# Kernel tuning notes

Hardware: AMD Instinct MI355X
Metric: run time of the kernel (lower is better)

Reference implementation:

```python
import jax, jax.numpy as jnp
import numpy as np

# Static config (matches init_kwargs)
B = 1
D = 1024          # model_dim
H = 16            # num_heads
HD = 64           # head_dim
TPF = 256         # tokens_per_frame = latent_height*latent_width
LH, LW = 16, 16
FRAMES = 13
PREFIX = 1
ATTN = 3
CHUNKS = 4
TXT = 226                 # text_length per chunk
SEQ_TXT = CHUNKS * TXT    # 904
VID_LEN = FRAMES * TPF    # 3328
CHUNK_VID = (PREFIX + ATTN) * TPF  # 1024 video tokens per attention chunk
THETA = 10000.0
EPS = 1e-6
SCALE = 1.0 / np.sqrt(HD)
DT, DHE, DW = 16, 24, 24  # 3D rope split of head_dim


def setup_inputs() -> dict:
    key = jax.random.key(0)
    ks = jax.random.split(key, 16)
    def w(k, shape, s=0.02):
        return (jax.random.normal(k, shape) * s).astype(jnp.float32)
    return dict(
        vid_emb=jax.random.normal(ks[0], (B, VID_LEN, D), jnp.float32),
        text_emb=jax.random.normal(ks[1], (B, SEQ_TXT, D), jnp.float32),
        Wq=w(ks[2], (D, D)), bq=jnp.zeros((D,), jnp.float32),
        Wk=w(ks[3], (D, D)), bk=jnp.zeros((D,), jnp.float32),
        Wv=w(ks[4], (D, D)), bv=jnp.zeros((D,), jnp.float32),
        Wo=w(ks[5], (D, D)), bo=jnp.zeros((D,), jnp.float32),
        qn_w=jnp.ones((HD,), jnp.float32), qn_b=jnp.zeros((HD,), jnp.float32),
        kn_w=jnp.ones((HD,), jnp.float32), kn_b=jnp.zeros((HD,), jnp.float32),
        ssm_Win=w(ks[6], (D, D)), ssm_Wout=w(ks[7], (D, D)),
        ssm_gate=jnp.zeros((D,), jnp.float32),
        fg_t=jnp.full((D,), 0.1, jnp.float32), fg_v=jnp.full((D,), 0.1, jnp.float32),
        bg_t=jnp.full((D,), 0.1, jnp.float32), bg_v=jnp.full((D,), 0.1, jnp.float32),
    )


def _layernorm(x, w, b):
    mu = jnp.mean(x, axis=-1, keepdims=True)
    var = jnp.mean((x - mu) ** 2, axis=-1, keepdims=True)
    return (x - mu) * jax.lax.rsqrt(var + EPS) * w + b


def _rope_angles():
    # per-video-token 3D positions within a chunk
    tok = jnp.arange(CHUNK_VID)
    f = (tok // TPF).astype(jnp.float32)
    rem = tok % TPF
    hp = (rem // LW).astype(jnp.float32)
    wp = (rem % LW).astype(jnp.float32)
    def inv(d):
        return THETA ** (-jnp.arange(0, d, 2, dtype=jnp.float32) / d)
    return f[:, None] * inv(DT), hp[:, None] * inv(DHE), wp[:, None] * inv(DW)


def _rot(x, ang):
    half = x.shape[-1] // 2
    c, s = jnp.cos(ang), jnp.sin(ang)
    x1, x2 = x[..., :half], x[..., half:]
    return jnp.concatenate([x1 * c - x2 * s, x1 * s + x2 * c], axis=-1)


def _apply_rope3d(x, angs):
    at, ah, aw = angs
    return jnp.concatenate([
        _rot(x[..., :DT], at),
        _rot(x[..., DT:DT + DHE], ah),
        _rot(x[..., DT + DHE:], aw),
    ], axis=-1)


def _attn_forward(vid_emb, text_emb, Wq, bq, Wk, bk, Wv, bv, Wo, bo, qn_w, qn_b, kn_w, kn_b):
    b = vid_emb.shape[0]
    starts = np.arange(CHUNKS) * ATTN * TPF
    idx = jnp.asarray(starts)[:, None] + jnp.arange(CHUNK_VID)[None, :]  # [C, CHUNK_VID]
    txt_chunks = text_emb.reshape(b, CHUNKS, TXT, D)
    vid_chunks = vid_emb[:, idx]                                          # [b, C, CHUNK_VID, D]
    cur = jnp.concatenate([txt_chunks, vid_chunks], axis=2)               # [b, C, T, D]
    T = TXT + CHUNK_VID
    cur = cur.reshape(b * CHUNKS, T, D)

    def heads(x):
        return x.reshape(b * CHUNKS, T, H, HD).transpose(0, 2, 1, 3)      # [bc, h, t, d]

    q = _layernorm(heads(cur @ Wq + bq), qn_w, qn_b)
    k = _layernorm(heads(cur @ Wk + bk), kn_w, kn_b)
    v = heads(cur @ Wv + bv)

    angs = _rope_angles()
    q = jnp.concatenate([q[:, :, :TXT], _apply_rope3d(q[:, :, TXT:], angs)], axis=2)
    k = jnp.concatenate([k[:, :, :TXT], _apply_rope3d(k[:, :, TXT:], angs)], axis=2)

    scores = jnp.einsum('bhqd,bhkd->bhqk', q, k) * SCALE
    attn = jax.nn.softmax(scores, axis=-1)
    out = jnp.einsum('bhqk,bhkd->bhqd', attn, v)
    out = out.transpose(0, 2, 1, 3).reshape(b * CHUNKS, T, D) @ Wo + bo
    out = out.reshape(b, CHUNKS, T, D)

    text_out = out[:, :, :TXT].reshape(b, SEQ_TXT, D)
    vid_part = out[:, :, TXT:]                                            # [b, C, CHUNK_VID, D]
    vid_acc = jnp.zeros((b, VID_LEN, D), vid_emb.dtype).at[:, idx].add(vid_part)
    cnt = jnp.zeros((b, VID_LEN, 1), vid_emb.dtype).at[:, idx].add(jnp.ones((b, CHUNKS, CHUNK_VID, 1), vid_emb.dtype))
    vid_out = vid_acc / cnt
    return jnp.concatenate([text_out, vid_out], axis=1)


def _ssm(x, Win, Wout, gate_logit):
    # simplified TTT stand-in: gated linear recurrence h_t = g*h_{t-1} + u_t (causal scan)
    g = jax.nn.sigmoid(gate_logit)
    u = x @ Win
    a = jnp.broadcast_to(g, u.shape)
    def comb(c1, c2):
        a1, b1 = c1
        a2, b2 = c2
        return a1 * a2, a2 * b1 + b2
    _, h = jax.lax.associative_scan(comb, (a, u), axis=1)
    return h @ Wout


def _rev_text_chunks(t):
    b = t.shape[0]
    return jnp.flip(t.reshape(b, CHUNKS, TXT, D), axis=1).reshape(b, SEQ_TXT, D)


def _ssm_forward(emb, ssm_Win, ssm_Wout, ssm_gate, fg_t, fg_v, bg_t, bg_v):
    Ttxt = SEQ_TXT
    res = emb
    y = _ssm(emb, ssm_Win, ssm_Wout, ssm_gate)
    emb = res + jnp.concatenate([jnp.tanh(fg_t) * y[:, :Ttxt], jnp.tanh(fg_v) * y[:, Ttxt:]], axis=1)
    res2 = emb
    # multiscene reverse: flip text chunk order and video token order
    rev = jnp.concatenate([_rev_text_chunks(emb[:, :Ttxt]), jnp.flip(emb[:, Ttxt:], axis=1)], axis=1)
    y2 = _ssm(rev, ssm_Win, ssm_Wout, ssm_gate)
    y2 = jnp.concatenate([_rev_text_chunks(y2[:, :Ttxt]), jnp.flip(y2[:, Ttxt:], axis=1)], axis=1)
    return res2 + jnp.concatenate([jnp.tanh(bg_t) * y2[:, :Ttxt], jnp.tanh(bg_v) * y2[:, Ttxt:]], axis=1)


def reference(vid_emb, text_emb, Wq, bq, Wk, bk, Wv, bv, Wo, bo, qn_w, qn_b, kn_w, kn_b,
              ssm_Win, ssm_Wout, ssm_gate, fg_t, fg_v, bg_t, bg_v):
    emb = _attn_forward(vid_emb, text_emb, Wq, bq, Wk, bk, Wv, bv, Wo, bo, qn_w, qn_b, kn_w, kn_b)
    out = _ssm_forward(emb, ssm_Win, ssm_Wout, ssm_gate, fg_t, fg_v, bg_t, bg_v)
    return out[:, SEQ_TXT:], out[:, :SEQ_TXT]
```

## Files before the change

kernel.cpp:

```cpp
#include <hip/hip_runtime.h>
#include <cstdint>

constexpr int Dm       = 1024;
constexpr int Hh       = 16;
constexpr int HD       = 64;
constexpr int CHUNKS   = 4;
constexpr int TXT      = 226;
constexpr int SEQ_TXT  = 904;
constexpr int VID_LEN  = 3328;
constexpr int CHUNK_VID= 1024;
constexpr int Tt       = 1250;
constexpr int Tp       = 1280;
constexpr int M_QKV    = 5000;
constexpr int SEQm     = 4232;
constexpr int STRIDE_V = 768;
constexpr float EPSc   = 1e-6f;
constexpr float SCALEc = 0.125f;
constexpr float OFFS   = 8.0f;
constexpr float C16    = 1.6609640474f;
constexpr float C24    = 1.1073093649f;

constexpr int SEGL2 = 64;
constexpr int HALO  = 64;
constexpr int NSEG2 = (SEQm + SEGL2 - 1) / SEGL2;

typedef __attribute__((ext_vector_type(8))) short bf16x8;
typedef __attribute__((ext_vector_type(4))) float f32x4;

__device__ __forceinline__ ushort f2bf(float x) {
    uint32_t u = __float_as_uint(x);
    u += 0x7FFFu + ((u >> 16) & 1u);
    return (ushort)(u >> 16);
}
__device__ __forceinline__ float bf2f(ushort b) {
    return __uint_as_float(((uint32_t)b) << 16);
}

__device__ __forceinline__ void gload_lds16(const ushort* g, ushort* l) {
    __builtin_amdgcn_global_load_lds(
        (const __attribute__((address_space(1))) unsigned int*)g,
        (__attribute__((address_space(3))) unsigned int*)l, 16, 0, 0);
}

__device__ __forceinline__ int rev_map(int i) {
    if (i < SEQ_TXT) {
        int c = i / TXT, o = i - c * TXT;
        return (CHUNKS - 1 - c) * TXT + o;
    }
    int j = i - SEQ_TXT;
    return SEQ_TXT + (VID_LEN - 1 - j);
}

__global__ __launch_bounds__(256) void prep_all(
    const float* __restrict__ Wq, const float* __restrict__ Wk,
    const float* __restrict__ Wv, const float* __restrict__ Wo,
    const float* __restrict__ Win, const float* __restrict__ Wout,
    const float* __restrict__ vid, const float* __restrict__ txt,
    ushort* __restrict__ WqkvH, ushort* __restrict__ WqkvL,
    ushort* __restrict__ WoH, ushort* __restrict__ WoL,
    ushort* __restrict__ WinH, ushort* __restrict__ WinL,
    ushort* __restrict__ WoutH, ushort* __restrict__ WoutL,
    ushort* __restrict__ chi, ushort* __restrict__ clo) {
    __shared__ float tile[32][33];
    if (blockIdx.z == 6) {
        int base = (blockIdx.y * 32 + blockIdx.x) * 256 + threadIdx.x;
        for (int idx = base; idx < M_QKV * 256; idx += 32 * 32 * 256) {
            int row = idx >> 8, c4 = (idx & 255) * 4;
            int c = row / Tt, t = row - c * Tt;
            float4 x;
            if (t < TXT)
                x = *(const float4*)(txt + (size_t)(c * TXT + t) * Dm + c4);
            else
                x = *(const float4*)(vid + (size_t)(c * STRIDE_V + (t - TXT)) * Dm + c4);
            float v[4] = {x.x, x.y, x.z, x.w};
            ushort4 h, l;
            h.x = f2bf(v[0]); l.x = f2bf(v[0] - bf2f(h.x));
            h.y = f2bf(v[1]); l.y = f2bf(v[1] - bf2f(h.y));
            h.z = f2bf(v[2]); l.z = f2bf(v[2] - bf2f(h.z));
            h.w = f2bf(v[3]); l.w = f2bf(v[3] - bf2f(h.w));
            *(ushort4*)(chi + (size_t)row * Dm + c4) = h;
            *(ushort4*)(clo + (size_t)row * Dm + c4) = l;
        }
        return;
    }
    const float* W; ushort* Thi; ushort* Tlo;
    switch (blockIdx.z) {
        case 0: W = Wq;  Thi = WqkvH;               Tlo = WqkvL;               break;
        case 1: W = Wk;  Thi = WqkvH + 1024*1024;   Tlo = WqkvL + 1024*1024;   break;
        case 2: W = Wv;  Thi = WqkvH + 2*1024*1024; Tlo = WqkvL + 2*1024*1024; break;
        case 3: W = Wo;  Thi = WoH;   Tlo = WoL;   break;
        case 4: W = Win; Thi = WinH;  Tlo = WinL;  break;
        default:W = Wout;Thi = WoutH; Tlo = WoutL; break;
    }
    int k0 = blockIdx.y * 32, n0 = blockIdx.x * 32;
    int j = threadIdx.x & 31, i0 = threadIdx.x >> 5;
#pragma unroll
    for (int i = i0; i < 32; i += 8)
        tile[i][j] = W[(size_t)(k0 + i) * 1024 + n0 + j];
    __syncthreads();
#pragma unroll
    for (int i = i0; i < 32; i += 8) {
        float v = tile[j][i];
        ushort h = f2bf(v);
        size_t o = (size_t)(n0 + i) * 1024 + k0 + j;
        Thi[o] = h;
        Tlo[o] = f2bf(v - bf2f(h));
    }
}

template<int MODE>
__global__ __launch_bounds__(256) void gemm_sk(
    const ushort* __restrict__ Ahi, const ushort* __restrict__ Alo,
    const ushort* __restrict__ Bhi, const ushort* __restrict__ Blo,
    const float* __restrict__ f1, const float* __restrict__ f2,
    const float* __restrict__ f3,
    float* __restrict__ Cf, ushort* __restrict__ u1,
    int M, int N) {
    __shared__ ushort AHL[128 * 64];
    __shared__ ushort BHL[128 * 64];
    const int tid = threadIdx.x;
    const int w = tid >> 6, lane = tid & 63;
    const int lrow = lane & 15, quad = lane >> 4;
    const int mBase = blockIdx.y * 128, nBase = blockIdx.x * 128;

    const bool isB = (w >= 2);
    const int half = w & 1;
    const ushort* Phi = isB ? Bhi : Ahi;
    const ushort* Plo = isB ? Blo : Alo;
    ushort* lds = (isB ? BHL : AHL) + half * 4096;
    const int baseR = (isB ? nBase : mBase) + half * 64;
    const int maxr = (isB ? N : M) - 1;
    const int rl8 = lane >> 3;
    const int c = (lane & 7) ^ rl8;
    const ushort* Psel = (c < 4) ? Phi : Plo;
    const ushort* gb[8];
#pragma unroll
    for (int u = 0; u < 8; ++u) {
        int rg = min(baseR + u * 8 + rl8, maxr);
        gb[u] = Psel + (size_t)rg * 1024 + (c & 3) * 8;
    }

    const int mo = (w >> 1) * 64, no = (w & 1) * 64;
    const int p = quad ^ (lrow & 7);
    f32x4 acc[4][4];
#pragma unroll
    for (int i = 0; i < 4; ++i)
#pragma unroll
        for (int j = 0; j < 4; ++j) acc[i][j] = (f32x4){0.f, 0.f, 0.f, 0.f};

    const int kk0 = (MODE == 5) ? blockIdx.z * 512 : 0;
    const int kk1 = (MODE == 5) ? kk0 + 512 : 1024;
    for (int kk = kk0; kk < kk1; kk += 32) {
        __syncthreads();
#pragma unroll
        for (int u = 0; u < 8; ++u) gload_lds16(gb[u] + kk, lds + u * 512);
        __syncthreads();

        bf16x8 ah[4], al[4], bh[4], bl[4];
#pragma unroll
        for (int i = 0; i < 4; ++i) {
            int m = mo + i * 16 + lrow;
            ah[i] = *(const bf16x8*)&AHL[m * 64 + p * 8];
            al[i] = *(const bf16x8*)&AHL[m * 64 + (p ^ 4) * 8];
        }
#pragma unroll
        for (int j = 0; j < 4; ++j) {
            int n = no + j * 16 + lrow;
            bh[j] = *(const bf16x8*)&BHL[n * 64 + p * 8];
            bl[j] = *(const bf16x8*)&BHL[n * 64 + (p ^ 4) * 8];
        }
#pragma unroll
        for (int i = 0; i < 4; ++i)
#pragma unroll
            for (int j = 0; j < 4; ++j) {
                f32x4 a = acc[i][j];
                a = __builtin_amdgcn_mfma_f32_16x16x32_bf16(ah[i], bh[j], a, 0, 0, 0);
                a = __builtin_amdgcn_mfma_f32_16x16x32_bf16(al[i], bh[j], a, 0, 0, 0);
                a = __builtin_amdgcn_mfma_f32_16x16x32_bf16(ah[i], bl[j], a, 0, 0, 0);
                acc[i][j] = a;
            }
    }

    const size_t zoff = (MODE == 5) ? (size_t)blockIdx.z * M * N : 0;
#pragma unroll
    for (int i = 0; i < 4; ++i)
#pragma unroll
        for (int j = 0; j < 4; ++j) {
            const int col = nBase + no + j * 16 + lrow;
            float bv = 0.f;
            if constexpr (MODE == 1)
                bv = (col < 1024) ? f1[col]
                   : (col < 2048) ? f2[col - 1024] : f3[col - 2048];
#pragma unroll
            for (int r = 0; r < 4; ++r) {
                const int row = mBase + mo + i * 16 + quad * 4 + r;
                if (row >= M) continue;
                const size_t idx = (size_t)row * N + col;
                const float a = acc[i][j][r];
                if constexpr (MODE == 1) {
                    u1[idx] = f2bf(a + bv);
                } else {
                    Cf[zoff + idx] = a;
                }
            }
        }
}

__global__ __launch_bounds__(512, 2) void gemm_qkv_8ph(
    const ushort* __restrict__ Ahi, const ushort* __restrict__ Alo,
    const ushort* __restrict__ Bhi, const ushort* __restrict__ Blo,
    const float* __restrict__ f1, const float* __restrict__ f2,
    const float* __restrict__ f3, ushort* __restrict__ out) {
    constexpr int Mq  = M_QKV;
    constexpr int Nq  = 3072;
    constexpr int NKT = 48;

    __shared__ __align__(16) ushort sA00[8192], sA01[8192];
    __shared__ __align__(16) ushort sA10[8192], sA11[8192];
    __shared__ __align__(16) ushort sB00[8192], sB01[8192];
    __shared__ __align__(16) ushort sB10[8192], sB11[8192];

    const int tid = threadIdx.x;
    const int w = tid >> 6, lane = tid & 63;
    const int lrow = lane & 15, quad = lane >> 4;
    const int wr = w >> 2, wc = w & 3;

    const int wg  = blockIdx.y * 12 + blockIdx.x;
    const int swz = (wg & 7) * 30 + (wg >> 3);
    const int bx  = swz % 12, by = swz / 12;
    const int mBase = by * 256, nBase = bx * 256;

    uint32_t offA[2][2], offB[2][2];
#pragma unroll
    for (int q = 0; q < 2; ++q) {
        const int s  = q * 512 + tid;
        const int sr = s >> 3;
        const int c  = (s & 7) ^ (sr & 7);
        const int ra = (sr >> 6) * 128 + (sr & 63);
        const int rb = (sr >> 5) * 64 + (sr & 31);
#pragma unroll
        for (int h = 0; h < 2; ++h) {
            offA[q][h] = (uint32_t)(min(mBase + ra + h * 64, Mq - 1) * 1024 + c * 8);
            offB[q][h] = (uint32_t)((nBase + rb + h * 32) * 1024 + c * 8);
        }
    }
    const int ldsW = w * 512;

    const int pA0 = quad ^ (lrow & 7);
    const int pA1 = (4 + quad) ^ (lrow & 7);
    const int arow = wr * 64 + lrow;
    const int brow = wc * 32 + lrow;

    f32x4 acc[8][4];
#pragma unroll
    for (int i = 0; i < 8; ++i)
#pragma unroll
        for (int j = 0; j < 4; ++j) acc[i][j] = (f32x4){0.f, 0.f, 0.f, 0.f};

    bf16x8 af[8];
    bf16x8 bfX[4];
    bf16x8 bfY[4];

#define STAGE_A(b, h, kt) do { \
        const ushort* pl_ = (((kt) >> 4) == 1 ? Alo : Ahi) + (((kt) & 15) * 64); \
        ushort* d_ = &sA##b##h[ldsW]; \
        gload_lds16(pl_ + offA[0][(h)], d_); \
        gload_lds16(pl_ + offA[1][(h)], d_ + 4096); \
    } while (0)
#define STAGE_B(b, h, kt) do { \
        const ushort* pl_ = (((kt) >> 4) == 2 ? Blo : Bhi) + (((kt) & 15) * 64); \
        ushort* d_ = &sB##b##h[ldsW]; \
        gload_lds16(pl_ + offB[0][(h)], d_); \
        gload_lds16(pl_ + offB[1][(h)], d_ + 4096); \
    } while (0)
#define LD_A(b, h) do { \
        const ushort* ba_ = sA##b##h; \
        af[0] = *(const bf16x8*)(ba_ + (arow +  0) * 64 + pA0 * 8); \
        af[1] = *(const bf16x8*)(ba_ + (arow +  0) * 64 + pA1 * 8); \
        af[2] = *(const bf16x8*)(ba_ + (arow + 16) * 64 + pA0 * 8); \
        af[3] = *(const bf16x8*)(ba_ + (arow + 16) * 64 + pA1 * 8); \
        af[4] = *(const bf16x8*)(ba_ + (arow + 32) * 64 + pA0 * 8); \
        af[5] = *(const bf16x8*)(ba_ + (arow + 32) * 64 + pA1 * 8); \
        af[6] = *(const bf16x8*)(ba_ + (arow + 48) * 64 + pA0 * 8); \
        af[7] = *(const bf16x8*)(ba_ + (arow + 48) * 64 + pA1 * 8); \
    } while (0)
#define LD_B(dst, b, h) do { \
        const ushort* bb_ = sB##b##h; \
        dst[0] = *(const bf16x8*)(bb_ + (brow +  0) * 64 + pA0 * 8); \
        dst[1] = *(const bf16x8*)(bb_ + (brow +  0) * 64 + pA1 * 8); \
        dst[2] = *(const bf16x8*)(bb_ + (brow + 16) * 64 + pA0 * 8); \
        dst[3] = *(const bf16x8*)(bb_ + (brow + 16) * 64 + pA1 * 8); \
    } while (0)
#define MMO(mh, nh, i, ks, B) \
        acc[(mh)*4+(i)][(nh)*2+0] = __builtin_amdgcn_mfma_f32_16x16x32_bf16( \
            af[(i)*2+(ks)], B[0+(ks)], acc[(mh)*4+(i)][(nh)*2+0], 0, 0, 0); \
        acc[(mh)*4+(i)][(nh)*2+1] = __builtin_amdgcn_mfma_f32_16x16x32_bf16( \
            af[(i)*2+(ks)], B[2+(ks)], acc[(mh)*4+(i)][(nh)*2+1], 0, 0, 0);
#define MM16(mh, nh, B) do { \
        __builtin_amdgcn_s_setprio(1); \
        MMO(mh, nh, 0, 0, B) MMO(mh, nh, 1, 0, B) MMO(mh, nh, 2, 0, B) MMO(mh, nh, 3, 0, B) \
        MMO(mh, nh, 0, 1, B) MMO(mh, nh, 1, 1, B) MMO(mh, nh, 2, 1, B) MMO(mh, nh, 3, 1, B) \
        __builtin_amdgcn_s_setprio(0); \
    } while (0)
#define BAR()  __builtin_amdgcn_s_barrier()
#define VMC4() asm volatile("s_waitcnt vmcnt(4)" ::: "memory")

    STAGE_A(0, 0, 0); STAGE_B(0, 1, 0); STAGE_B(0, 0, 0); STAGE_A(0, 1, 0);
    STAGE_A(1, 0, 1); STAGE_B(1, 1, 1);
    VMC4();
    BAR();

#pragma unroll 1
    for (int t = 0; t < NKT / 2; ++t) {
        const int kt1  = 2 * t + 1;
        const int ktn0 = min(2 * t + 2, NKT - 1);
        const int ktn1 = min(2 * t + 3, NKT - 1);
        LD_A(0, 0); LD_B(bfX, 0, 0);
        STAGE_B(1, 0, kt1);
        BAR();
        MM16(0, 0, bfX);
        BAR();
        LD_B(bfY, 0, 1);
        STAGE_A(1, 1, kt1);
        BAR();
        MM16(0, 1, bfY);
        BAR();
        LD_A(0, 1);
        STAGE_A(0, 0, ktn0);
        BAR();
        MM16(1, 1, bfY);
        BAR();
        STAGE_B(0, 1, ktn0);
        BAR();
        MM16(1, 0, bfX);
        VMC4();
        BAR();
        LD_A(1, 0); LD_B(bfX, 1, 0);
        STAGE_B(0, 0, ktn0);
        BAR();
        MM16(0, 0, bfX);
        BAR();
        LD_B(bfY, 1, 1);
        STAGE_A(0, 1, ktn0);
        BAR();
        MM16(0, 1, bfY);
        BAR();
        LD_A(1, 1);
        STAGE_A(1, 0, ktn1);
        BAR();
        MM16(1, 1, bfY);
        BAR();
        STAGE_B(1, 1, ktn1);
        BAR();
        MM16(1, 0, bfX);
        VMC4();
        BAR();
    }
    asm volatile("s_waitcnt vmcnt(0)" ::: "memory");

#undef STAGE_A
#undef STAGE_B
#undef LD_A
#undef LD_B
#undef MMO
#undef MM16
#undef BAR
#undef VMC4

#pragma unroll
    for (int i = 0; i < 8; ++i) {
#pragma unroll
        for (int j = 0; j < 4; ++j) {
            const int col = nBase + wc * 64 + j * 16 + lrow;
            const float bias = (col < 1024) ? f1[col]
                             : (col < 2048) ? f2[col - 1024] : f3[col - 2048];
#pragma unroll
            for (int r = 0; r < 4; ++r) {
                const int row = mBase + wr * 128 + i * 16 + quad * 4 + r;
                if (row < Mq)
                    out[(size_t)row * Nq + col] = f2bf(acc[i][j][r] + bias);
            }
        }
    }
}

__global__ __launch_bounds__(256) void lnrope(
    const ushort* __restrict__ qkvb,
    const float* __restrict__ qn_w, const float* __restrict__ qn_b,
    const float* __restrict__ kn_w, const float* __restrict__ kn_b,
    ushort* __restrict__ qP, ushort* __restrict__ kP, ushort* __restrict__ vT) {
    __shared__ ushort vtile[64][72];
    const int ch = blockIdx.y, c = ch >> 4, h = ch & 15;
    const int t0 = blockIdx.x * 64;
    const int tid = threadIdx.x, w = tid >> 6, lane = tid & 63;

    auto wsum = [](float x) {
#pragma unroll
        for (int o = 32; o; o >>= 1) x += __shfl_xor(x, o);
        return x;
    };

#pragma unroll 1
    for (int it = 0; it < 16; ++it) {
        const int tl = w * 16 + it;
        const int t = t0 + tl;
        ushort qb = 0, kb = 0, vb = 0;
        if (t < Tt) {
            size_t src = (size_t)(c * Tt + t) * 3072 + h * HD + lane;
            float qv = bf2f(qkvb[src]);
            float kv = bf2f(qkvb[src + 1024]);
            float vv = bf2f(qkvb[src + 2048]);

            float qmu = wsum(qv) * (1.f / 64.f);
            float qd  = qv - qmu;
            float qvar = wsum(qd * qd) * (1.f / 64.f);
            float qn = qd * rsqrtf(qvar + EPSc) * qn_w[lane] + qn_b[lane];

            float kmu = wsum(kv) * (1.f / 64.f);
            float kd  = kv - kmu;
            float kvar = wsum(kd * kd) * (1.f / 64.f);
            float kn = kd * rsqrtf(kvar + EPSc) * kn_w[lane] + kn_b[lane];

            if (t >= TXT) {
                int pos = t - TXT;
                int f = pos >> 8, rem2 = pos & 255, hp = rem2 >> 4, wp = rem2 & 15;
                int p, dl; float cc;
                if (lane < 16)      { cc = C16; p = f;  dl = lane; }
                else if (lane < 40) { cc = C24; p = hp; dl = lane - 16; }
                else                { cc = C24; p = wp; dl = lane - 40; }
                int halfd = (lane < 16) ? 8 : 12;
                int i = (dl < halfd) ? dl : dl - halfd;
                float ang = (float)p * exp2f(-(float)i * cc);
                float cs = cosf(ang), sn = sinf(ang);
                int partner = (dl < halfd) ? (lane + halfd) : (lane - halfd);
                float qo = __shfl(qn, partner);
                float ko = __shfl(kn, partner);
                qn = (dl < halfd) ? (qn * cs - qo * sn) : (qo * sn + qn * cs);
                kn = (dl < halfd) ? (kn * cs - ko * sn) : (ko * sn + kn * cs);
            }
            qb = f2bf(qn * SCALEc);
            kb = f2bf(kn);
            vb = f2bf(vv);
        }
        size_t dst = ((size_t)ch * Tp + t) * HD + lane;
        qP[dst] = qb;
        kP[dst] = kb;
        vtile[tl][lane] = vb;
    }
    __syncthreads();
    const int r = tid >> 2, ck = tid & 3;
    ushort* dst = vT + ((size_t)ch * HD + r) * Tp + t0;
    short o1[8], o2[8];
#pragma unroll
    for (int j = 0; j < 8; ++j) {
        o1[j] = (short)vtile[ck * 8 + j][r];
        o2[j] = (short)vtile[(ck + 4) * 8 + j][r];
    }
    *(bf16x8*)(dst + ck * 8)       = *(bf16x8*)o1;
    *(bf16x8*)(dst + (ck + 4) * 8) = *(bf16x8*)o2;
}

__global__ __launch_bounds__(256) void attn_mfma(
    const ushort* __restrict__ qP, const ushort* __restrict__ kP,
    const ushort* __restrict__ vT,
    ushort* __restrict__ ohi, ushort* __restrict__ olo) {
    const int ch = blockIdx.y;
    const int c = ch >> 4, h = ch & 15;
    const int qbase = blockIdx.x * 64;
    const int tid = threadIdx.x, w = tid >> 6, lane = tid & 63;
    const int lrow = lane & 15, quad = lane >> 4;

    __shared__ ushort KT[2][32 * 64];
    __shared__ ushort VTs[2][64 * 32];
    __shared__ ushort PB[4][16][40];

    const ushort* kg = kP + (size_t)ch * Tp * HD;
    const ushort* vg = vT + (size_t)ch * HD * Tp;

    const ushort* kgl = kg + (size_t)(w * 8 + (lane >> 3)) * HD
                           + ((lane & 7) ^ ((lane >> 3) & 7)) * 8;
    const ushort* vgl = vg + (size_t)(w * 16 + (lane >> 2)) * Tp + (lane & 3) * 8;

    const int qr = qbase + w * 16 + lrow;
    const ushort* qgp = qP + ((size_t)ch * Tp + qr) * HD + quad * 8;
    bf16x8 qf0 = *(const bf16x8*)qgp;
    bf16x8 qf1 = *(const bf16x8*)(qgp + 32);

    f32x4 accO[4];
#pragma unroll
    for (int dt = 0; dt < 4; ++dt) accO[dt] = (f32x4){0.f, 0.f, 0.f, 0.f};
    float lacc[4] = {0.f, 0.f, 0.f, 0.f};

    gload_lds16(kgl, &KT[0][w * 512]);
    gload_lds16(vgl, &VTs[0][w * 512]);

    const int NSTEP = Tp / 32;
    for (int s = 0; s < NSTEP; ++s) {
        const int b = s & 1;
        __syncthreads();
        if (s + 1 < NSTEP) {
            int kb = (s + 1) * 32;
            gload_lds16(kgl + (size_t)kb * HD, &KT[1 - b][w * 512]);
            gload_lds16(vgl + kb, &VTs[1 - b][w * 512]);
        }

        const int sw = lrow & 7;
        const ushort* r0 = &KT[b][lrow * 64];
        const ushort* r1 = &KT[b][(16 + lrow) * 64];
        bf16x8 k00 = *(const bf16x8*)(r0 + (quad ^ sw) * 8);
        bf16x8 k01 = *(const bf16x8*)(r0 + ((4 + quad) ^ sw) * 8);
        bf16x8 k10 = *(const bf16x8*)(r1 + (quad ^ sw) * 8);
        bf16x8 k11 = *(const bf16x8*)(r1 + ((4 + quad) ^ sw) * 8);
        f32x4 s0 = (f32x4){0.f, 0.f, 0.f, 0.f}, s1 = s0;
        s0 = __builtin_amdgcn_mfma_f32_16x16x32_bf16(qf0, k00, s0, 0, 0, 0);
        s0 = __builtin_amdgcn_mfma_f32_16x16x32_bf16(qf1, k01, s0, 0, 0, 0);
        s1 = __builtin_amdgcn_mfma_f32_16x16x32_bf16(qf0, k10, s1, 0, 0, 0);
        s1 = __builtin_amdgcn_mfma_f32_16x16x32_bf16(qf1, k11, s1, 0, 0, 0);

#pragma unroll
        for (int r = 0; r < 4; ++r) {
            float p0 = __expf(s0[r] - OFFS);
            float p1 = __expf(s1[r] - OFFS);
            lacc[r] += p0 + p1;
            int row = quad * 4 + r;
            PB[w][row][lrow]      = f2bf(p0);
            PB[w][row][16 + lrow] = f2bf(p1);
        }

        bf16x8 pf = *(const bf16x8*)&PB[w][lrow][quad * 8];
#pragma unroll
        for (int dt = 0; dt < 4; ++dt) {
            bf16x8 vf = *(const bf16x8*)&VTs[b][(dt * 16 + lrow) * 32 + quad * 8];
            accO[dt] = __builtin_amdgcn_mfma_f32_16x16x32_bf16(pf, vf, accO[dt], 0, 0, 0);
        }
    }

    float il[4];
#pragma unroll
    for (int r = 0; r < 4; ++r) {
        float l = lacc[r];
        l += __shfl_xor(l, 1);
        l += __shfl_xor(l, 2);
        l += __shfl_xor(l, 4);
        l += __shfl_xor(l, 8);
        l -= (float)(Tp - Tt) * __expf(-OFFS);
        il[r] = 1.f / l;
    }
#pragma unroll
    for (int dt = 0; dt < 4; ++dt)
#pragma unroll
        for (int r = 0; r < 4; ++r) {
            int qrow = qbase + w * 16 + quad * 4 + r;
            if (qrow < Tt) {
                float val = accO[dt][r] * il[r];
                size_t o = (size_t)(c * Tt + qrow) * Dm + h * HD + dt * 16 + lrow;
                ushort hv = f2bf(val);
                ohi[o] = hv;
                olo[o] = f2bf(val - bf2f(hv));
            }
        }
}

__global__ __launch_bounds__(256) void reduce_scatter(
    const float* __restrict__ P0, const float* __restrict__ bo,
    ushort* __restrict__ ehi, ushort* __restrict__ elo) {
    const float* P1 = P0 + (size_t)M_QKV * Dm;
    int idx = blockIdx.x * 256 + threadIdx.x;
    int row = idx >> 8, c4 = (idx & 255) * 4;
    float sx, sy, sz, sw;
    if (row < SEQ_TXT) {
        int c = row / TXT, t = row - c * TXT;
        size_t o = (size_t)(c * Tt + t) * Dm + c4;
        float4 a = *(const float4*)(P0 + o);
        float4 b = *(const float4*)(P1 + o);
        sx = a.x + b.x; sy = a.y + b.y; sz = a.z + b.z; sw = a.w + b.w;
    } else {
        int p = row - SEQ_TXT;
        sx = sy = sz = sw = 0.f; int cnt = 0;
#pragma unroll
        for (int c = 0; c < CHUNKS; ++c) {
            int off = p - c * STRIDE_V;
            if (off >= 0 && off < CHUNK_VID) {
                size_t o = (size_t)(c * Tt + TXT + off) * Dm + c4;
                float4 a = *(const float4*)(P0 + o);
                float4 b = *(const float4*)(P1 + o);
                sx += a.x + b.x; sy += a.y + b.y;
                sz += a.z + b.z; sw += a.w + b.w;
                ++cnt;
            }
        }
        float inv = 1.f / (float)cnt;
        sx *= inv; sy *= inv; sz *= inv; sw *= inv;
    }
    float4 b4 = *(const float4*)(bo + c4);
    float v[4] = {sx + b4.x, sy + b4.y, sz + b4.z, sw + b4.w};
    ushort4 h, l;
    h.x = f2bf(v[0]); l.x = f2bf(v[0] - bf2f(h.x));
    h.y = f2bf(v[1]); l.y = f2bf(v[1] - bf2f(h.y));
    h.z = f2bf(v[2]); l.z = f2bf(v[2] - bf2f(h.z));
    h.w = f2bf(v[3]); l.w = f2bf(v[3] - bf2f(h.w));
    *(ushort4*)(ehi + (size_t)row * Dm + c4) = h;
    *(ushort4*)(elo + (size_t)row * Dm + c4) = l;
}

__global__ __launch_bounds__(256) void scan_halo(
    const float* __restrict__ P0, const float* __restrict__ gate,
    ushort* __restrict__ hhi, ushort* __restrict__ hlo, int perm) {
    const float* P1 = P0 + (size_t)SEQm * Dm;
    int ch = blockIdx.x * 256 + threadIdx.x;
    int seg = blockIdx.y;
    float g = 1.f / (1.f + expf(-gate[ch]));
    int tw0 = seg * SEGL2;
    int tw1 = min(SEQm, tw0 + SEGL2);
    int t0 = max(0, tw0 - HALO);
    float hv = 0.f;
    for (int t = t0; t < tw0; ++t) {
        int rt = perm ? rev_map(t) : t;
        size_t o = (size_t)rt * Dm + ch;
        hv = fmaf(g, hv, P0[o] + P1[o]);
    }
    for (int t = tw0; t < tw1; ++t) {
        int rt = perm ? rev_map(t) : t;
        size_t o = (size_t)rt * Dm + ch;
        hv = fmaf(g, hv, P0[o] + P1[o]);
        ushort h = f2bf(hv);
        hhi[o] = h;
        hlo[o] = f2bf(hv - bf2f(h));
    }
}

__global__ __launch_bounds__(256) void reduce_c1(
    const float* __restrict__ P0,
    const ushort* __restrict__ ehi, const ushort* __restrict__ elo,
    const float* __restrict__ fg_t, const float* __restrict__ fg_v,
    float* __restrict__ emb2, ushort* __restrict__ e2hi, ushort* __restrict__ e2lo) {
    const float* P1 = P0 + (size_t)SEQm * Dm;
    int idx = blockIdx.x * 256 + threadIdx.x;
    int row = idx >> 8, c4 = (idx & 255) * 4;
    const float* fg = (row < SEQ_TXT) ? fg_t : fg_v;
    size_t o = (size_t)row * Dm + c4;
    float4 a = *(const float4*)(P0 + o);
    float4 b = *(const float4*)(P1 + o);
    ushort4 eh = *(const ushort4*)(ehi + o);
    ushort4 el = *(const ushort4*)(elo + o);
    float v[4];
    v[0] = (bf2f(eh.x) + bf2f(el.x)) + tanhf(fg[c4 + 0]) * (a.x + b.x);
    v[1] = (bf2f(eh.y) + bf2f(el.y)) + tanhf(fg[c4 + 1]) * (a.y + b.y);
    v[2] = (bf2f(eh.z) + bf2f(el.z)) + tanhf(fg[c4 + 2]) * (a.z + b.z);
    v[3] = (bf2f(eh.w) + bf2f(el.w)) + tanhf(fg[c4 + 3]) * (a.w + b.w);
    *(float4*)(emb2 + o) = make_float4(v[0], v[1], v[2], v[3]);
    ushort4 h, l;
    h.x = f2bf(v[0]); l.x = f2bf(v[0] - bf2f(h.x));
    h.y = f2bf(v[1]); l.y = f2bf(v[1] - bf2f(h.y));
    h.z = f2bf(v[2]); l.z = f2bf(v[2] - bf2f(h.z));
    h.w = f2bf(v[3]); l.w = f2bf(v[3] - bf2f(h.w));
    *(ushort4*)(e2hi + o) = h;
    *(ushort4*)(e2lo + o) = l;
}

__global__ __launch_bounds__(256) void reduce_fin(
    const float* __restrict__ P0, const float* __restrict__ emb2,
    const float* __restrict__ bg_t, const float* __restrict__ bg_v,
    float* __restrict__ outp) {
    const float* P1 = P0 + (size_t)SEQm * Dm;
    int idx = blockIdx.x * 256 + threadIdx.x;
    int row = idx >> 8, c4 = (idx & 255) * 4;
    const float* bg = (row < SEQ_TXT) ? bg_t : bg_v;
    int drow = (row >= SEQ_TXT) ? (row - SEQ_TXT) : (VID_LEN + row);
    size_t o = (size_t)row * Dm + c4;
    float4 a = *(const float4*)(P0 + o);
    float4 b = *(const float4*)(P1 + o);
    float4 e = *(const float4*)(emb2 + o);
    float4 r = make_float4(e.x + tanhf(bg[c4 + 0]) * (a.x + b.x),
                           e.y + tanhf(bg[c4 + 1]) * (a.y + b.y),
                           e.z + tanhf(bg[c4 + 2]) * (a.z + b.z),
                           e.w + tanhf(bg[c4 + 3]) * (a.w + b.w));
    *(float4*)(outp + (size_t)drow * Dm + c4) = r;
}

extern "C" void kernel_launch(void* const* d_in, const int* in_sizes, int n_in,
                              void* d_out, int out_size, void* d_ws, size_t ws_size,
                              hipStream_t stream) {
    const float* vid_emb = (const float*)d_in[0];
    const float* text_emb= (const float*)d_in[1];
    const float* Wq = (const float*)d_in[2];  const float* bq = (const float*)d_in[3];
    const float* Wk = (const float*)d_in[4];  const float* bk = (const float*)d_in[5];
    const float* Wv = (const float*)d_in[6];  const float* bv = (const float*)d_in[7];
    const float* Wo = (const float*)d_in[8];  const float* bo = (const float*)d_in[9];
    const float* qn_w = (const float*)d_in[10]; const float* qn_b = (const float*)d_in[11];
    const float* kn_w = (const float*)d_in[12]; const float* kn_b = (const float*)d_in[13];
    const float* Win  = (const float*)d_in[14]; const float* Wout = (const float*)d_in[15];
    const float* gate = (const float*)d_in[16];
    const float* fg_t = (const float*)d_in[17]; const float* fg_v = (const float*)d_in[18];
    const float* bg_t = (const float*)d_in[19]; const float* bg_v = (const float*)d_in[20];

    char* W8 = (char*)d_ws;
    if (ws_size < 128647168u) return;
    ushort* WqkvH = (ushort*)(W8 + 0);
    ushort* WqkvL = (ushort*)(W8 + 6291456);
    ushort* WoH   = (ushort*)(W8 + 12582912);
    ushort* WoL   = (ushort*)(W8 + 14680064);
    ushort* WinH  = (ushort*)(W8 + 16777216);
    ushort* WinL  = (ushort*)(W8 + 18874368);
    ushort* WoutH = (ushort*)(W8 + 20971520);
    ushort* WoutL = (ushort*)(W8 + 23068672);
    ushort* qkvb  = (ushort*)(W8 + 25165824);
    ushort* curH  = (ushort*)(W8 + 55885824);
    ushort* curL  = (ushort*)(W8 + 66125824);
    ushort* qPl   = (ushort*)(W8 + 76365824);
    ushort* kPl   = (ushort*)(W8 + 86851584);
    ushort* vTl   = (ushort*)(W8 + 97337344);
    ushort* aoutH = (ushort*)(W8 + 25165824);
    ushort* aoutL = (ushort*)(W8 + 35405824);
    float*  PWo   = (float*) (W8 + 76365824);
    ushort* embH  = (ushort*)(W8 + 45645824);
    ushort* embL  = (ushort*)(W8 + 54312960);
    float*  PW    = (float*) (W8 + 76365824);
    ushort* hbufH = (ushort*)(W8 + 25165824);
    ushort* hbufL = (ushort*)(W8 + 33832960);
    float*  emb2  = (float*) (W8 + 111034368);
    ushort* e2H   = (ushort*)(W8 + 25165824);
    ushort* e2L   = (ushort*)(W8 + 33832960);
    ushort* hbuf2H= (ushort*)(W8 + 45645824);
    ushort* hbuf2L= (ushort*)(W8 + 54312960);
    float*  outp  = (float*)d_out;

    prep_all<<<dim3(32, 32, 7), 256, 0, stream>>>(
        Wq, Wk, Wv, Wo, Win, Wout, vid_emb, text_emb,
        WqkvH, WqkvL, WoH, WoL, WinH, WinL, WoutH, WoutL, curH, curL);

    gemm_qkv_8ph<<<dim3(12, 20), 512, 0, stream>>>(
        curH, curL, WqkvH, WqkvL, bq, bk, bv, qkvb);

    lnrope<<<dim3(Tp / 64, 64), 256, 0, stream>>>(qkvb, qn_w, qn_b, kn_w, kn_b,
                                                  qPl, kPl, vTl);

    attn_mfma<<<dim3(Tp / 64, 64), 256, 0, stream>>>(qPl, kPl, vTl, aoutH, aoutL);

    gemm_sk<5><<<dim3(8, 40, 2), 256, 0, stream>>>(
        aoutH, aoutL, WoH, WoL, nullptr, nullptr, nullptr, PWo, nullptr,
        M_QKV, 1024);
    reduce_scatter<<<SEQm, 256, 0, stream>>>(PWo, bo, embH, embL);

    dim3 gsq(8, 34, 2);
    dim3 gscan(Dm / 256, NSEG2);

    gemm_sk<5><<<gsq, 256, 0, stream>>>(
        embH, embL, WinH, WinL, nullptr, nullptr, nullptr, PW, nullptr,
        SEQm, 1024);
    scan_halo<<<gscan, 256, 0, stream>>>(PW, gate, hbufH, hbufL, 0);
    gemm_sk<5><<<gsq, 256, 0, stream>>>(
        hbufH, hbufL, WoutH, WoutL, nullptr, nullptr, nullptr, PW, nullptr,
        SEQm, 1024);
    reduce_c1<<<SEQm, 256, 0, stream>>>(PW, embH, embL, fg_t, fg_v,
                                        emb2, e2H, e2L);

    gemm_sk<5><<<gsq, 256, 0, stream>>>(
        e2H, e2L, WinH, WinL, nullptr, nullptr, nullptr, PW, nullptr,
        SEQm, 1024);
    scan_halo<<<gscan, 256, 0, stream>>>(PW, gate, hbuf2H, hbuf2L, 1);
    gemm_sk<5><<<gsq, 256, 0, stream>>>(
        hbuf2H, hbuf2L, WoutH, WoutL, nullptr, nullptr, nullptr, PW, nullptr,
        SEQm, 1024);
    reduce_fin<<<SEQm, 256, 0, stream>>>(PW, emb2, bg_t, bg_v, outp);
}
```

Measured before the change: 669.7 us.

## Restructure QKV GEMM pipeline into four phases with merged LDS buffer

Reorganises the 8-phase QKV GEMM main loop into 4 coarser phases, each issuing two LDS fragment loads and two global-to-LDS stages before a single barrier, then running two MFMA blocks back to back. The goal is to halve the number of workgroup barriers per K step and to raise instruction priority only around the MFMA blocks. It also merges the eight separate LDS arrays into one buffer and drops the L2-oriented workgroup swizzle in favour of plain block indexing. The new ordering relies on explicit lgkmcnt waits, which may expose LDS latency, and dropping the swizzle may reduce cache locality.

```diff
diff --git a/kernel.cpp b/kernel.cpp
--- a/kernel.cpp
+++ b/kernel.cpp
@@ -215,20 +215,14 @@
     constexpr int Nq  = 3072;
     constexpr int NKT = 48;
 
-    __shared__ __align__(16) ushort sA00[8192], sA01[8192];
-    __shared__ __align__(16) ushort sA10[8192], sA11[8192];
-    __shared__ __align__(16) ushort sB00[8192], sB01[8192];
-    __shared__ __align__(16) ushort sB10[8192], sB11[8192];
+    __shared__ __align__(16) ushort ldsq[65536];
 
     const int tid = threadIdx.x;
     const int w = tid >> 6, lane = tid & 63;
     const int lrow = lane & 15, quad = lane >> 4;
     const int wr = w >> 2, wc = w & 3;
 
-    const int wg  = blockIdx.y * 12 + blockIdx.x;
-    const int swz = (wg & 7) * 30 + (wg >> 3);
-    const int bx  = swz % 12, by = swz / 12;
-    const int mBase = by * 256, nBase = bx * 256;
+    const int mBase = blockIdx.y * 256, nBase = blockIdx.x * 256;
 
     uint32_t offA[2][2], offB[2][2];
 #pragma unroll
@@ -261,20 +255,22 @@
     bf16x8 bfX[4];
     bf16x8 bfY[4];
 
+#define A_LDS(b, h) (ldsq + ((b) * 2 + (h)) * 8192)
+#define B_LDS(b, h) (ldsq + 32768 + ((b) * 2 + (h)) * 8192)
 #define STAGE_A(b, h, kt) do { \
         const ushort* pl_ = (((kt) >> 4) == 1 ? Alo : Ahi) + (((kt) & 15) * 64); \
-        ushort* d_ = &sA##b##h[ldsW]; \
+        ushort* d_ = A_LDS(b, h) + ldsW; \
         gload_lds16(pl_ + offA[0][(h)], d_); \
         gload_lds16(pl_ + offA[1][(h)], d_ + 4096); \
     } while (0)
 #define STAGE_B(b, h, kt) do { \
         const ushort* pl_ = (((kt) >> 4) == 2 ? Blo : Bhi) + (((kt) & 15) * 64); \
-        ushort* d_ = &sB##b##h[ldsW]; \
+        ushort* d_ = B_LDS(b, h) + ldsW; \
         gload_lds16(pl_ + offB[0][(h)], d_); \
         gload_lds16(pl_ + offB[1][(h)], d_ + 4096); \
     } while (0)
 #define LD_A(b, h) do { \
-        const ushort* ba_ = sA##b##h; \
+        const ushort* ba_ = A_LDS(b, h); \
         af[0] = *(const bf16x8*)(ba_ + (arow +  0) * 64 + pA0 * 8); \
         af[1] = *(const bf16x8*)(ba_ + (arow +  0) * 64 + pA1 * 8); \
         af[2] = *(const bf16x8*)(ba_ + (arow + 16) * 64 + pA0 * 8); \
@@ -285,7 +281,7 @@
         af[7] = *(const bf16x8*)(ba_ + (arow + 48) * 64 + pA1 * 8); \
     } while (0)
 #define LD_B(dst, b, h) do { \
-        const ushort* bb_ = sB##b##h; \
+        const ushort* bb_ = B_LDS(b, h); \
         dst[0] = *(const bf16x8*)(bb_ + (brow +  0) * 64 + pA0 * 8); \
         dst[1] = *(const bf16x8*)(bb_ + (brow +  0) * 64 + pA1 * 8); \
         dst[2] = *(const bf16x8*)(bb_ + (brow + 16) * 64 + pA0 * 8); \
@@ -297,13 +293,14 @@
         acc[(mh)*4+(i)][(nh)*2+1] = __builtin_amdgcn_mfma_f32_16x16x32_bf16( \
             af[(i)*2+(ks)], B[2+(ks)], acc[(mh)*4+(i)][(nh)*2+1], 0, 0, 0);
 #define MM16(mh, nh, B) do { \
-        __builtin_amdgcn_s_setprio(1); \
         MMO(mh, nh, 0, 0, B) MMO(mh, nh, 1, 0, B) MMO(mh, nh, 2, 0, B) MMO(mh, nh, 3, 0, B) \
         MMO(mh, nh, 0, 1, B) MMO(mh, nh, 1, 1, B) MMO(mh, nh, 2, 1, B) MMO(mh, nh, 3, 1, B) \
-        __builtin_amdgcn_s_setprio(0); \
     } while (0)
 #define BAR()  __builtin_amdgcn_s_barrier()
+#define LGK0() asm volatile("s_waitcnt lgkmcnt(0)" ::: "memory")
 #define VMC4() asm volatile("s_waitcnt vmcnt(4)" ::: "memory")
+#define PRIO1() __builtin_amdgcn_s_setprio(1)
+#define PRIO0() __builtin_amdgcn_s_setprio(0)
 
     STAGE_A(0, 0, 0); STAGE_B(0, 1, 0); STAGE_B(0, 0, 0); STAGE_A(0, 1, 0);
     STAGE_A(1, 0, 1); STAGE_B(1, 1, 1);
@@ -315,49 +312,33 @@
         const int kt1  = 2 * t + 1;
         const int ktn0 = min(2 * t + 2, NKT - 1);
         const int ktn1 = min(2 * t + 3, NKT - 1);
-        LD_A(0, 0); LD_B(bfX, 0, 0);
-        STAGE_B(1, 0, kt1);
-        BAR();
-        MM16(0, 0, bfX);
-        BAR();
-        LD_B(bfY, 0, 1);
-        STAGE_A(1, 1, kt1);
-        BAR();
-        MM16(0, 1, bfY);
+        LD_A(0, 0); LD_B(bfX, 0, 0); LD_B(bfY, 0, 1);
+        STAGE_B(1, 0, kt1); STAGE_A(1, 1, kt1);
+        BAR(); LGK0();
+        PRIO1(); MM16(0, 0, bfX); MM16(0, 1, bfY); PRIO0();
         BAR();
         LD_A(0, 1);
-        STAGE_A(0, 0, ktn0);
-        BAR();
-        MM16(1, 1, bfY);
-        BAR();
-        STAGE_B(0, 1, ktn0);
-        BAR();
-        MM16(1, 0, bfX);
+        STAGE_A(0, 0, ktn0); STAGE_B(0, 1, ktn0);
+        BAR(); LGK0();
+        PRIO1(); MM16(1, 1, bfY); MM16(1, 0, bfX); PRIO0();
         VMC4();
         BAR();
-        LD_A(1, 0); LD_B(bfX, 1, 0);
-        STAGE_B(0, 0, ktn0);
-        BAR();
-        MM16(0, 0, bfX);
-        BAR();
-        LD_B(bfY, 1, 1);
-        STAGE_A(0, 1, ktn0);
-        BAR();
-        MM16(0, 1, bfY);
+        LD_A(1, 0); LD_B(bfX, 1, 0); LD_B(bfY, 1, 1);
+        STAGE_B(0, 0, ktn0); STAGE_A(0, 1, ktn0);
+        BAR(); LGK0();
+        PRIO1(); MM16(0, 0, bfX); MM16(0, 1, bfY); PRIO0();
         BAR();
         LD_A(1, 1);
-        STAGE_A(1, 0, ktn1);
-        BAR();
-        MM16(1, 1, bfY);
-        BAR();
-        STAGE_B(1, 1, ktn1);
-        BAR();
-        MM16(1, 0, bfX);
+        STAGE_A(1, 0, ktn1); STAGE_B(1, 1, ktn1);
+        BAR(); LGK0();
+        PRIO1(); MM16(1, 1, bfY); MM16(1, 0, bfX); PRIO0();
         VMC4();
         BAR();
     }
     asm volatile("s_waitcnt vmcnt(0)" ::: "memory");
 
+#undef A_LDS
+#undef B_LDS
 #undef STAGE_A
 #undef STAGE_B
 #undef LD_A
@@ -365,7 +346,10 @@
 #undef MMO
 #undef MM16
 #undef BAR
+#undef LGK0
 #undef VMC4
+#undef PRIO1
+#undef PRIO0
 
 #pragma unroll
     for (int i = 0; i < 8; ++i) {
```

Result: no change. 661.4 us (-1.2%).
